# Kernel optimization log

Hardware: AMD Instinct MI355X
Metric: run time of the kernel (lower is better)

Reference implementation:

```python
import jax, jax.numpy as jnp
import numpy as np

STATE_DIM = 1024
INPUT_DIM = 1024
BATCH = 8192


def setup_inputs() -> dict:
    key = jax.random.key(0)
    ks = jax.random.split(key, 7)
    # Kaiming-uniform-ish init like torch Linear
    bx = 1.0 / np.sqrt(INPUT_DIM)
    bh = 1.0 / np.sqrt(STATE_DIM)
    return {
        "x": jax.random.normal(ks[0], (BATCH, INPUT_DIM), jnp.float32),
        "prevh": jax.random.normal(ks[1], (BATCH, STATE_DIM), jnp.float32),
        "prevc": jax.random.normal(ks[2], (BATCH, STATE_DIM), jnp.float32),
        "Wx": jax.random.uniform(ks[3], (INPUT_DIM, 4 * STATE_DIM), jnp.float32, -bx, bx),
        "bx": jax.random.uniform(ks[4], (4 * STATE_DIM,), jnp.float32, -bx, bx),
        "Wh": jax.random.uniform(ks[5], (STATE_DIM, 4 * STATE_DIM), jnp.float32, -bh, bh),
    }


def reference(x, prevh, prevc, Wx, bx, Wh):
    # stacked gate pre-activations: [B, 4*state_dim]
    stacked = x @ Wx + bx + prevh @ Wh
    i_bar, f_bar, o_bar, g_bar = jnp.split(stacked, 4, axis=1)
    i = jax.nn.sigmoid(i_bar)
    f = jax.nn.sigmoid(f_bar)
    o = jax.nn.sigmoid(o_bar)
    g = jnp.tanh(g_bar)
    nextc = prevc * f + g * i
    nexth = jnp.tanh(nextc) * o
    return (nexth, nextc)
```

## Files before the change

### kernel.cpp

```cpp
#include <hip/hip_runtime.h>
#include <hip/hip_bf16.h>


#define BATCH   8192
#define SDIM    1024
#define KDIM    2048
#define NT      32

typedef __attribute__((ext_vector_type(8))) short s16x8;
typedef __attribute__((ext_vector_type(4))) float f32x4;

__device__ __forceinline__ void gload16(const void* g, void* l) {
    __builtin_amdgcn_global_load_lds((const __attribute__((address_space(1))) void*)g,
                                     (__attribute__((address_space(3))) void*)l,
                                     16, 0, 0);
}

__device__ __forceinline__ float fast_sigmoid(float x) {
    return 1.0f / (1.0f + __expf(-x));
}
__device__ __forceinline__ float fast_tanh(float v) {
    float a = fabsf(v);
    float e = __expf(-2.0f * a);
    float t = (1.0f - e) / (1.0f + e);
    return copysignf(t, v);
}

__global__ __launch_bounds__(256) void convAW(
    const float* __restrict__ x,  const float* __restrict__ h,
    const float* __restrict__ Wx, const float* __restrict__ Wh,
    __hip_bfloat16* __restrict__ A, __hip_bfloat16* __restrict__ Wt)
{
    __shared__ float tile[64][68];
    if (blockIdx.x < 8192) {
        int t = blockIdx.x * 256 + threadIdx.x;
        int e = t << 3;
        int b = e >> 11;
        int k = e & 2047;
        const float* src = (k < 1024) ? (x + (size_t)b * 1024 + k)
                                      : (h + (size_t)b * 1024 + (k - 1024));
        float4 v0 = *(const float4*)(src);
        float4 v1 = *(const float4*)(src + 4);
        union { __hip_bfloat16 b[8]; s16x8 v; } u;
        u.b[0] = __float2bfloat16(v0.x); u.b[1] = __float2bfloat16(v0.y);
        u.b[2] = __float2bfloat16(v0.z); u.b[3] = __float2bfloat16(v0.w);
        u.b[4] = __float2bfloat16(v1.x); u.b[5] = __float2bfloat16(v1.y);
        u.b[6] = __float2bfloat16(v1.z); u.b[7] = __float2bfloat16(v1.w);
        *(s16x8*)(A + e) = u.v;
    } else {
        const int wb = blockIdx.x - 8192;
        const int kt = wb & 31;
        const int nt = wb >> 5;
        const int k0 = kt * 64, n0 = nt * 64;
        const int t  = threadIdx.x;

        {
            int r = t >> 2;
            int c = (t & 3) * 16;
            int k = k0 + r;
            const float* src = (k < 1024) ? (Wx + (size_t)k * 4096 + n0 + c)
                                          : (Wh + (size_t)(k - 1024) * 4096 + n0 + c);
#pragma unroll
            for (int jq = 0; jq < 4; ++jq)
                *(float4*)&tile[r][c + jq * 4] = *(const float4*)(src + jq * 4);
        }
        __syncthreads();

#pragma unroll
        for (int it = 0; it < 2; ++it) {
            int item = t + it * 256;
            int oct  = item >> 6;
            int nl   = item & 63;
            int n    = n0 + nl;
            int s    = n & 1023, g = n >> 10;
            int np   = (s >> 4) * 64 + g * 16 + (s & 15);
            union { __hip_bfloat16 b[8]; s16x8 v; } u;
#pragma unroll
            for (int e = 0; e < 8; ++e)
                u.b[e] = __float2bfloat16(tile[oct * 8 + e][nl]);
            *(s16x8*)(Wt + (size_t)np * 2048 + k0 + oct * 8) = u.v;
        }
    }
}

__global__ __launch_bounds__(512, 2) void lstm_gemm(
    const __hip_bfloat16* __restrict__ A,
    const __hip_bfloat16* __restrict__ Wt,
    const float* __restrict__ bx,
    const float* __restrict__ prevc,
    float* __restrict__ outh,
    float* __restrict__ outc)
{
    __shared__ __align__(16) char lds[131072];

    const int tid  = threadIdx.x;
    const int lane = tid & 63;
    const int w    = tid >> 6;
    const int wr   = w >> 2;
    const int wc   = w & 3;
    const int l15  = lane & 15;

    const int bid = blockIdx.x;
    const int xcd = bid & 7, j = bid >> 3;
    const int mt = (xcd >> 1) * 8 + (j & 7);
    const int nt = (xcd & 1) * 8 + (j >> 3);
    const int m0 = mt * 256, n0 = nt * 256, S0 = nt * 64;

    const int scol = ((lane & 7) ^ (lane >> 3)) << 3;
    const __hip_bfloat16* Ag = A  + (size_t)m0 * KDIM;
    const __hip_bfloat16* Bg = Wt + (size_t)n0 * KDIM;

    auto SA = [&](int tt, int p) {
        char* dst = lds + (2 * (tt & 1) + p) * 16384 + w * 1024;
        const __hip_bfloat16* src =
            Ag + (size_t)(p * 128 + w * 8 + (lane >> 3)) * KDIM + tt * 64 + scol;
        gload16(src, dst);
        gload16(src + (size_t)64 * KDIM, dst + 8192);
    };
    auto SB = [&](int tt, int p) {
        char* dst = lds + 65536 + (2 * (tt & 1) + p) * 16384 + w * 1024;
        const __hip_bfloat16* src =
            Bg + (size_t)(p * 128 + w * 8 + (lane >> 3)) * KDIM + tt * 64 + scol;
        gload16(src, dst);
        gload16(src + (size_t)64 * KDIM, dst + 8192);
    };

    f32x4 acc[8][4];
#pragma unroll
    for (int m = 0; m < 8; ++m)
#pragma unroll
        for (int g = 0; g < 4; ++g)
            acc[m][g] = (f32x4)0.0f;

    SB(0, 0); SB(0, 1); SA(0, 0); SA(0, 1); SB(1, 0); SB(1, 1);
    asm volatile("s_waitcnt vmcnt(4)" ::: "memory");
    __builtin_amdgcn_s_barrier();
    __builtin_amdgcn_sched_barrier(0);

    const int swz0 = (((lane >> 4))     ^ (lane & 7)) << 4;
    const int swz1 = (((lane >> 4) | 4) ^ (lane & 7)) << 4;
    const int brow = (wc & 1) * 64;

    s16x8 af[4][2], bf[4][2];

    for (int t = 0; t < NT; ++t) {
        const char* as = lds + (2 * (t & 1) + wr) * 16384;
        const char* bs = lds + 65536 + (2 * (t & 1) + (wc >> 1)) * 16384;

#pragma unroll
        for (int g = 0; g < 4; ++g) {
            bf[g][0] = *(const s16x8*)(bs + (brow + g * 16 + l15) * 128 + swz0);
            bf[g][1] = *(const s16x8*)(bs + (brow + g * 16 + l15) * 128 + swz1);
        }
#pragma unroll
        for (int m = 0; m < 4; ++m) {
            af[m][0] = *(const s16x8*)(as + (m * 16 + l15) * 128 + swz0);
            af[m][1] = *(const s16x8*)(as + (m * 16 + l15) * 128 + swz1);
        }
        if (t + 1 < NT) { SA(t + 1, 0); SA(t + 1, 1); }

        __builtin_amdgcn_s_setprio(1);
#pragma unroll
        for (int kf = 0; kf < 2; ++kf)
#pragma unroll
            for (int m = 0; m < 4; ++m)
#pragma unroll
                for (int g = 0; g < 4; ++g)
                    acc[m][g] = __builtin_amdgcn_mfma_f32_16x16x32_bf16(
                        af[m][kf], bf[g][kf], acc[m][g], 0, 0, 0);
        __builtin_amdgcn_s_setprio(0);

        __builtin_amdgcn_sched_barrier(0);
        __builtin_amdgcn_s_barrier();
        __builtin_amdgcn_sched_barrier(0);

#pragma unroll
        for (int m = 0; m < 4; ++m) {
            af[m][0] = *(const s16x8*)(as + ((m + 4) * 16 + l15) * 128 + swz0);
            af[m][1] = *(const s16x8*)(as + ((m + 4) * 16 + l15) * 128 + swz1);
        }
        if (t + 2 < NT) { SB(t + 2, 0); SB(t + 2, 1); }

        __builtin_amdgcn_s_setprio(1);
#pragma unroll
        for (int kf = 0; kf < 2; ++kf)
#pragma unroll
            for (int m = 0; m < 4; ++m)
#pragma unroll
                for (int g = 0; g < 4; ++g)
                    acc[m + 4][g] = __builtin_amdgcn_mfma_f32_16x16x32_bf16(
                        af[m][kf], bf[g][kf], acc[m + 4][g], 0, 0, 0);
        __builtin_amdgcn_s_setprio(0);

        __builtin_amdgcn_sched_barrier(0);
        if (t + 2 < NT) {
            asm volatile("s_waitcnt vmcnt(4)" ::: "memory");
        } else {
            asm volatile("s_waitcnt vmcnt(0)" ::: "memory");
        }
        __builtin_amdgcn_s_barrier();
        __builtin_amdgcn_sched_barrier(0);
    }

    const int st  = S0 + wc * 16 + l15;
    const float b_i = bx[st];
    const float b_f = bx[1024 + st];
    const float b_o = bx[2048 + st];
    const float b_g = bx[3072 + st];
    const int rbase = m0 + wr * 128 + (lane >> 4) * 4;

#pragma unroll
    for (int m = 0; m < 8; ++m) {
#pragma unroll
        for (int q = 0; q < 4; ++q) {
            int row = rbase + m * 16 + q;
            float ib = acc[m][0][q] + b_i;
            float fb = acc[m][1][q] + b_f;
            float ob = acc[m][2][q] + b_o;
            float gb = acc[m][3][q] + b_g;
            float ig = fast_sigmoid(ib);
            float fg = fast_sigmoid(fb);
            float og = fast_sigmoid(ob);
            float gg = fast_tanh(gb);
            float pc = prevc[(size_t)row * SDIM + st];
            float nc = pc * fg + gg * ig;
            float nh = fast_tanh(nc) * og;
            outh[(size_t)row * SDIM + st] = nh;
            outc[(size_t)row * SDIM + st] = nc;
        }
    }
}

extern "C" void kernel_launch(void* const* d_in, const int* in_sizes, int n_in,
                              void* d_out, int out_size, void* d_ws, size_t ws_size,
                              hipStream_t stream) {
    const float* x     = (const float*)d_in[0];
    const float* prevh = (const float*)d_in[1];
    const float* prevc = (const float*)d_in[2];
    const float* Wx    = (const float*)d_in[3];
    const float* bx    = (const float*)d_in[4];
    const float* Wh    = (const float*)d_in[5];

    __hip_bfloat16* Abf = (__hip_bfloat16*)d_ws;
    __hip_bfloat16* Wt  = Abf + (size_t)BATCH * KDIM;

    float* outh = (float*)d_out;
    float* outc = outh + (size_t)BATCH * SDIM;

    hipLaunchKernelGGL(convAW, dim3(10240), dim3(256), 0, stream,
                       x, prevh, Wx, Wh, Abf, Wt);
    hipLaunchKernelGGL(lstm_gemm, dim3(512), dim3(512), 0, stream,
                       Abf, Wt, bx, prevc, outh, outc);
}
```

Measured before the change: 156.1 us.

## Fuse activation fp32-to-bf16 conversion into GEMM A-tile loading

Drops the separate pass that converted x and prevh to a bf16 workspace matrix. The GEMM now loads fp32 activations straight into registers, converts them to bf16 and writes them into swizzled LDS, with the wait counts reorganised around this. This avoids writing and re-reading the 32MB bf16 copy of A. In exchange, A loads go through registers instead of direct global-to-LDS loads, fetch twice the bytes per tile (fp32) from global memory, and add conversion VALU work and extra waits inside the main loop.

```diff
diff --git a/kernel.cpp b/kernel.cpp
--- a/kernel.cpp
+++ b/kernel.cpp
@@ -26,65 +26,57 @@
     return copysignf(t, v);
 }
 
-__global__ __launch_bounds__(256) void convAW(
-    const float* __restrict__ x,  const float* __restrict__ h,
+__device__ __forceinline__ s16x8 cvt8(float4 a, float4 b) {
+    union { __hip_bfloat16 h[8]; s16x8 v; } u;
+    u.h[0] = __float2bfloat16(a.x); u.h[1] = __float2bfloat16(a.y);
+    u.h[2] = __float2bfloat16(a.z); u.h[3] = __float2bfloat16(a.w);
+    u.h[4] = __float2bfloat16(b.x); u.h[5] = __float2bfloat16(b.y);
+    u.h[6] = __float2bfloat16(b.z); u.h[7] = __float2bfloat16(b.w);
+    return u.v;
+}
+
+__global__ __launch_bounds__(256) void convW(
     const float* __restrict__ Wx, const float* __restrict__ Wh,
-    __hip_bfloat16* __restrict__ A, __hip_bfloat16* __restrict__ Wt)
+    __hip_bfloat16* __restrict__ Wt)
 {
     __shared__ float tile[64][68];
-    if (blockIdx.x < 8192) {
-        int t = blockIdx.x * 256 + threadIdx.x;
-        int e = t << 3;
-        int b = e >> 11;
-        int k = e & 2047;
-        const float* src = (k < 1024) ? (x + (size_t)b * 1024 + k)
-                                      : (h + (size_t)b * 1024 + (k - 1024));
-        float4 v0 = *(const float4*)(src);
-        float4 v1 = *(const float4*)(src + 4);
+    const int wb = blockIdx.x;
+    const int kt = wb & 31;
+    const int nt = wb >> 5;
+    const int k0 = kt * 64, n0 = nt * 64;
+    const int t  = threadIdx.x;
+
+    {
+        int r = t >> 2;
+        int c = (t & 3) * 16;
+        int k = k0 + r;
+        const float* src = (k < 1024) ? (Wx + (size_t)k * 4096 + n0 + c)
+                                      : (Wh + (size_t)(k - 1024) * 4096 + n0 + c);
+#pragma unroll
+        for (int jq = 0; jq < 4; ++jq)
+            *(float4*)&tile[r][c + jq * 4] = *(const float4*)(src + jq * 4);
+    }
+    __syncthreads();
+
+#pragma unroll
+    for (int it = 0; it < 2; ++it) {
+        int item = t + it * 256;
+        int oct  = item >> 6;
+        int nl   = item & 63;
+        int n    = n0 + nl;
+        int s    = n & 1023, g = n >> 10;
+        int np   = (s >> 4) * 64 + g * 16 + (s & 15);
         union { __hip_bfloat16 b[8]; s16x8 v; } u;
-        u.b[0] = __float2bfloat16(v0.x); u.b[1] = __float2bfloat16(v0.y);
-        u.b[2] = __float2bfloat16(v0.z); u.b[3] = __float2bfloat16(v0.w);
-        u.b[4] = __float2bfloat16(v1.x); u.b[5] = __float2bfloat16(v1.y);
-        u.b[6] = __float2bfloat16(v1.z); u.b[7] = __float2bfloat16(v1.w);
-        *(s16x8*)(A + e) = u.v;
-    } else {
-        const int wb = blockIdx.x - 8192;
-        const int kt = wb & 31;
-        const int nt = wb >> 5;
-        const int k0 = kt * 64, n0 = nt * 64;
-        const int t  = threadIdx.x;
-
-        {
-            int r = t >> 2;
-            int c = (t & 3) * 16;
-            int k = k0 + r;
-            const float* src = (k < 1024) ? (Wx + (size_t)k * 4096 + n0 + c)
-                                          : (Wh + (size_t)(k - 1024) * 4096 + n0 + c);
-#pragma unroll
-            for (int jq = 0; jq < 4; ++jq)
-                *(float4*)&tile[r][c + jq * 4] = *(const float4*)(src + jq * 4);
-        }
-        __syncthreads();
-
-#pragma unroll
-        for (int it = 0; it < 2; ++it) {
-            int item = t + it * 256;
-            int oct  = item >> 6;
-            int nl   = item & 63;
-            int n    = n0 + nl;
-            int s    = n & 1023, g = n >> 10;
-            int np   = (s >> 4) * 64 + g * 16 + (s & 15);
-            union { __hip_bfloat16 b[8]; s16x8 v; } u;
-#pragma unroll
-            for (int e = 0; e < 8; ++e)
-                u.b[e] = __float2bfloat16(tile[oct * 8 + e][nl]);
-            *(s16x8*)(Wt + (size_t)np * 2048 + k0 + oct * 8) = u.v;
-        }
+#pragma unroll
+        for (int e = 0; e < 8; ++e)
+            u.b[e] = __float2bfloat16(tile[oct * 8 + e][nl]);
+        *(s16x8*)(Wt + (size_t)np * 2048 + k0 + oct * 8) = u.v;
     }
 }
 
 __global__ __launch_bounds__(512, 2) void lstm_gemm(
-    const __hip_bfloat16* __restrict__ A,
+    const float* __restrict__ x,
+    const float* __restrict__ prevh,
     const __hip_bfloat16* __restrict__ Wt,
     const float* __restrict__ bx,
     const float* __restrict__ prevc,
@@ -107,16 +99,16 @@
     const int m0 = mt * 256, n0 = nt * 256, S0 = nt * 64;
 
     const int scol = ((lane & 7) ^ (lane >> 3)) << 3;
-    const __hip_bfloat16* Ag = A  + (size_t)m0 * KDIM;
     const __hip_bfloat16* Bg = Wt + (size_t)n0 * KDIM;
-
-    auto SA = [&](int tt, int p) {
-        char* dst = lds + (2 * (tt & 1) + p) * 16384 + w * 1024;
-        const __hip_bfloat16* src =
-            Ag + (size_t)(p * 128 + w * 8 + (lane >> 3)) * KDIM + tt * 64 + scol;
-        gload16(src, dst);
-        gload16(src + (size_t)64 * KDIM, dst + 8192);
+    const float* xg = x     + (size_t)m0 * 1024;
+    const float* hg = prevh + (size_t)m0 * 1024;
+    const int arow = w * 8 + (lane >> 3);
+
+    auto aptr = [&](int row, int tt) -> const float* {
+        return (tt < 16) ? xg + (size_t)row * 1024 + tt * 64 + scol
+                         : hg + (size_t)row * 1024 + (tt - 16) * 64 + scol;
     };
+
     auto SB = [&](int tt, int p) {
         char* dst = lds + 65536 + (2 * (tt & 1) + p) * 16384 + w * 1024;
         const __hip_bfloat16* src =
@@ -132,8 +124,36 @@
         for (int g = 0; g < 4; ++g)
             acc[m][g] = (f32x4)0.0f;
 
-    SB(0, 0); SB(0, 1); SA(0, 0); SA(0, 1); SB(1, 0); SB(1, 1);
-    asm volatile("s_waitcnt vmcnt(4)" ::: "memory");
+    float4 a00a, a00b, a01a, a01b, a10a, a10b, a11a, a11b;
+
+#define ALOAD(TT)                                                   \
+    {                                                               \
+        const float* q0 = aptr(arow, TT);                           \
+        const float* q1 = q0 + (size_t)64 * 1024;                   \
+        const float* q2 = aptr(arow + 128, TT);                     \
+        const float* q3 = q2 + (size_t)64 * 1024;                   \
+        a00a = *(const float4*)q0; a00b = *(const float4*)(q0 + 4); \
+        a01a = *(const float4*)q1; a01b = *(const float4*)(q1 + 4); \
+        a10a = *(const float4*)q2; a10b = *(const float4*)(q2 + 4); \
+        a11a = *(const float4*)q3; a11b = *(const float4*)(q3 + 4); \
+    }
+
+#define AWRITE(TT)                                                  \
+    {                                                               \
+        char* d0 = lds + (2 * ((TT) & 1)) * 16384 + w * 1024 + lane * 16; \
+        *(s16x8*)d0          = cvt8(a00a, a00b);                    \
+        *(s16x8*)(d0 + 8192) = cvt8(a01a, a01b);                    \
+        char* d1 = d0 + 16384;                                      \
+        *(s16x8*)d1          = cvt8(a10a, a10b);                    \
+        *(s16x8*)(d1 + 8192) = cvt8(a11a, a11b);                    \
+    }
+
+    ALOAD(0);
+    SB(0, 0); SB(0, 1); SB(1, 0); SB(1, 1);
+    asm volatile("s_waitcnt vmcnt(8)" ::: "memory");
+    __builtin_amdgcn_sched_barrier(0);
+    AWRITE(0);
+    asm volatile("s_waitcnt vmcnt(4) lgkmcnt(0)" ::: "memory");
     __builtin_amdgcn_s_barrier();
     __builtin_amdgcn_sched_barrier(0);
 
@@ -157,7 +177,7 @@
             af[m][0] = *(const s16x8*)(as + (m * 16 + l15) * 128 + swz0);
             af[m][1] = *(const s16x8*)(as + (m * 16 + l15) * 128 + swz1);
         }
-        if (t + 1 < NT) { SA(t + 1, 0); SA(t + 1, 1); }
+        if (t + 1 < NT) ALOAD(t + 1);
 
         __builtin_amdgcn_s_setprio(1);
 #pragma unroll
@@ -181,6 +201,16 @@
         }
         if (t + 2 < NT) { SB(t + 2, 0); SB(t + 2, 1); }
 
+        if (t + 2 < NT) {
+            asm volatile("s_waitcnt vmcnt(4)" ::: "memory");
+        } else if (t + 1 < NT) {
+            asm volatile("s_waitcnt vmcnt(0)" ::: "memory");
+        } else {
+            asm volatile("s_waitcnt vmcnt(0)" ::: "memory");
+        }
+        __builtin_amdgcn_sched_barrier(0);
+        if (t + 1 < NT) AWRITE(t + 1);
+
         __builtin_amdgcn_s_setprio(1);
 #pragma unroll
         for (int kf = 0; kf < 2; ++kf)
@@ -193,14 +223,12 @@
         __builtin_amdgcn_s_setprio(0);
 
         __builtin_amdgcn_sched_barrier(0);
-        if (t + 2 < NT) {
-            asm volatile("s_waitcnt vmcnt(4)" ::: "memory");
-        } else {
-            asm volatile("s_waitcnt vmcnt(0)" ::: "memory");
-        }
+        asm volatile("s_waitcnt lgkmcnt(0)" ::: "memory");
         __builtin_amdgcn_s_barrier();
         __builtin_amdgcn_sched_barrier(0);
     }
+#undef ALOAD
+#undef AWRITE
 
     const int st  = S0 + wc * 16 + l15;
     const float b_i = bx[st];
@@ -241,14 +269,12 @@
     const float* bx    = (const float*)d_in[4];
     const float* Wh    = (const float*)d_in[5];
 
-    __hip_bfloat16* Abf = (__hip_bfloat16*)d_ws;
-    __hip_bfloat16* Wt  = Abf + (size_t)BATCH * KDIM;
+    __hip_bfloat16* Wt = (__hip_bfloat16*)d_ws;
 
     float* outh = (float*)d_out;
     float* outc = outh + (size_t)BATCH * SDIM;
 
-    hipLaunchKernelGGL(convAW, dim3(10240), dim3(256), 0, stream,
-                       x, prevh, Wx, Wh, Abf, Wt);
+    hipLaunchKernelGGL(convW, dim3(2048), dim3(256), 0, stream, Wx, Wh, Wt);
     hipLaunchKernelGGL(lstm_gemm, dim3(512), dim3(512), 0, stream,
-                       Abf, Wt, bx, prevc, outh, outc);
-}
+                       x, prevh, Wt, bx, prevc, outh, outc);
+}
```

Measured after the change: 179.7 us. 15.1% more time.

## Shrink GEMM tile to 128x128 with K-step 32 and 256-thread blocks

Applied to the files above, without the earlier changes.

Replaces the 256x256 tile, 512-thread, K=64 GEMM with a 128x128 tile, 4 waves, K=32 per step and 32KB LDS. The grid grows to 2048 blocks with up to 3 blocks per CU, trading the larger tile's data reuse for occupancy and a simpler double-buffer pipeline. Each step now waits for all outstanding global loads before its barrier, which may expose load latency, and the smaller tile doubles the total traffic of A and W into LDS.

```diff
diff --git a/kernel.cpp b/kernel.cpp
--- a/kernel.cpp
+++ b/kernel.cpp
@@ -5,7 +5,7 @@
 #define BATCH   8192
 #define SDIM    1024
 #define KDIM    2048
-#define NT      32
+#define NT      64
 
 typedef __attribute__((ext_vector_type(8))) short s16x8;
 typedef __attribute__((ext_vector_type(4))) float f32x4;
@@ -53,7 +53,6 @@
         const int nt = wb >> 5;
         const int k0 = kt * 64, n0 = nt * 64;
         const int t  = threadIdx.x;
-
         {
             int r = t >> 2;
             int c = (t & 3) * 16;
@@ -65,7 +64,6 @@
                 *(float4*)&tile[r][c + jq * 4] = *(const float4*)(src + jq * 4);
         }
         __syncthreads();
-
 #pragma unroll
         for (int it = 0; it < 2; ++it) {
             int item = t + it * 256;
@@ -83,7 +81,7 @@
     }
 }
 
-__global__ __launch_bounds__(512, 2) void lstm_gemm(
+__global__ __launch_bounds__(256, 3) void lstm_gemm(
     const __hip_bfloat16* __restrict__ A,
     const __hip_bfloat16* __restrict__ Wt,
     const float* __restrict__ bx,
@@ -91,126 +89,101 @@
     float* __restrict__ outh,
     float* __restrict__ outc)
 {
-    __shared__ __align__(16) char lds[131072];
+    __shared__ __align__(16) char lds[32768];
 
     const int tid  = threadIdx.x;
     const int lane = tid & 63;
     const int w    = tid >> 6;
-    const int wr   = w >> 2;
-    const int wc   = w & 3;
+    const int wr   = w >> 1;
+    const int wc   = w & 1;
     const int l15  = lane & 15;
 
     const int bid = blockIdx.x;
     const int xcd = bid & 7, j = bid >> 3;
-    const int mt = (xcd >> 1) * 8 + (j & 7);
-    const int nt = (xcd & 1) * 8 + (j >> 3);
-    const int m0 = mt * 256, n0 = nt * 256, S0 = nt * 64;
-
-    const int scol = ((lane & 7) ^ (lane >> 3)) << 3;
+    const int mt  = (xcd >> 1) * 16 + (j & 15);
+    const int ntl = (xcd & 1) * 16 + (j >> 4);
+    const int m0  = mt * 128, n0 = ntl * 128;
+
+    const int gl    = (lane & 7) ^ (lane >> 3);
+    const int gl_hi = gl >> 2;
+    const int gl_k  = (gl & 3) * 8;
     const __hip_bfloat16* Ag = A  + (size_t)m0 * KDIM;
     const __hip_bfloat16* Bg = Wt + (size_t)n0 * KDIM;
 
-    auto SA = [&](int tt, int p) {
-        char* dst = lds + (2 * (tt & 1) + p) * 16384 + w * 1024;
-        const __hip_bfloat16* src =
-            Ag + (size_t)(p * 128 + w * 8 + (lane >> 3)) * KDIM + tt * 64 + scol;
-        gload16(src, dst);
-        gload16(src + (size_t)64 * KDIM, dst + 8192);
+    auto SA = [&](int tt) {
+        char* dst = lds + (tt & 1) * 8192 + w * 1024;
+#pragma unroll
+        for (int r = 0; r < 2; ++r) {
+            int row = 2 * (r * 32 + w * 8 + (lane >> 3)) + gl_hi;
+            gload16(Ag + (size_t)row * KDIM + tt * 32 + gl_k, dst + r * 4096);
+        }
     };
-    auto SB = [&](int tt, int p) {
-        char* dst = lds + 65536 + (2 * (tt & 1) + p) * 16384 + w * 1024;
-        const __hip_bfloat16* src =
-            Bg + (size_t)(p * 128 + w * 8 + (lane >> 3)) * KDIM + tt * 64 + scol;
-        gload16(src, dst);
-        gload16(src + (size_t)64 * KDIM, dst + 8192);
+    auto SB = [&](int tt) {
+        char* dst = lds + 16384 + (tt & 1) * 8192 + w * 1024;
+#pragma unroll
+        for (int r = 0; r < 2; ++r) {
+            int row = 2 * (r * 32 + w * 8 + (lane >> 3)) + gl_hi;
+            gload16(Bg + (size_t)row * KDIM + tt * 32 + gl_k, dst + r * 4096);
+        }
     };
 
-    f32x4 acc[8][4];
-#pragma unroll
-    for (int m = 0; m < 8; ++m)
+    f32x4 acc[4][4];
+#pragma unroll
+    for (int m = 0; m < 4; ++m)
 #pragma unroll
         for (int g = 0; g < 4; ++g)
             acc[m][g] = (f32x4)0.0f;
 
-    SB(0, 0); SB(0, 1); SA(0, 0); SA(0, 1); SB(1, 0); SB(1, 1);
-    asm volatile("s_waitcnt vmcnt(4)" ::: "memory");
+    SA(0); SB(0);
+    asm volatile("s_waitcnt vmcnt(0)" ::: "memory");
     __builtin_amdgcn_s_barrier();
     __builtin_amdgcn_sched_barrier(0);
 
-    const int swz0 = (((lane >> 4))     ^ (lane & 7)) << 4;
-    const int swz1 = (((lane >> 4) | 4) ^ (lane & 7)) << 4;
-    const int brow = (wc & 1) * 64;
-
-    s16x8 af[4][2], bf[4][2];
+    const int rdoff = ((l15 >> 1) << 7)
+                    + (((((l15 & 1) << 2) | (lane >> 4)) ^ (l15 >> 1)) << 4);
+    const int abase = wr * 32 * 128;
+    const int bbase = wc * 32 * 128;
+
+    s16x8 af[4], bf[4];
 
     for (int t = 0; t < NT; ++t) {
-        const char* as = lds + (2 * (t & 1) + wr) * 16384;
-        const char* bs = lds + 65536 + (2 * (t & 1) + (wc >> 1)) * 16384;
-
-#pragma unroll
-        for (int g = 0; g < 4; ++g) {
-            bf[g][0] = *(const s16x8*)(bs + (brow + g * 16 + l15) * 128 + swz0);
-            bf[g][1] = *(const s16x8*)(bs + (brow + g * 16 + l15) * 128 + swz1);
-        }
-#pragma unroll
-        for (int m = 0; m < 4; ++m) {
-            af[m][0] = *(const s16x8*)(as + (m * 16 + l15) * 128 + swz0);
-            af[m][1] = *(const s16x8*)(as + (m * 16 + l15) * 128 + swz1);
-        }
-        if (t + 1 < NT) { SA(t + 1, 0); SA(t + 1, 1); }
-
+        const char* as = lds + (t & 1) * 8192;
+        const char* bs = lds + 16384 + (t & 1) * 8192;
+
+#pragma unroll
+        for (int g = 0; g < 4; ++g)
+            bf[g] = *(const s16x8*)(bs + bbase + g * 1024 + rdoff);
+#pragma unroll
+        for (int m = 0; m < 4; ++m)
+            af[m] = *(const s16x8*)(as + abase + m * 1024 + rdoff);
+
+        if (t + 1 < NT) { SA(t + 1); SB(t + 1); }
+
+        asm volatile("s_waitcnt lgkmcnt(0)" ::: "memory");
+        __builtin_amdgcn_sched_barrier(0);
         __builtin_amdgcn_s_setprio(1);
 #pragma unroll
-        for (int kf = 0; kf < 2; ++kf)
-#pragma unroll
-            for (int m = 0; m < 4; ++m)
-#pragma unroll
-                for (int g = 0; g < 4; ++g)
-                    acc[m][g] = __builtin_amdgcn_mfma_f32_16x16x32_bf16(
-                        af[m][kf], bf[g][kf], acc[m][g], 0, 0, 0);
+        for (int m = 0; m < 4; ++m)
+#pragma unroll
+            for (int g = 0; g < 4; ++g)
+                acc[m][g] = __builtin_amdgcn_mfma_f32_16x16x32_bf16(
+                    af[m], bf[g], acc[m][g], 0, 0, 0);
         __builtin_amdgcn_s_setprio(0);
 
-        __builtin_amdgcn_sched_barrier(0);
-        __builtin_amdgcn_s_barrier();
-        __builtin_amdgcn_sched_barrier(0);
-
-#pragma unroll
-        for (int m = 0; m < 4; ++m) {
-            af[m][0] = *(const s16x8*)(as + ((m + 4) * 16 + l15) * 128 + swz0);
-            af[m][1] = *(const s16x8*)(as + ((m + 4) * 16 + l15) * 128 + swz1);
-        }
-        if (t + 2 < NT) { SB(t + 2, 0); SB(t + 2, 1); }
-
-        __builtin_amdgcn_s_setprio(1);
-#pragma unroll
-        for (int kf = 0; kf < 2; ++kf)
-#pragma unroll
-            for (int m = 0; m < 4; ++m)
-#pragma unroll
-                for (int g = 0; g < 4; ++g)
-                    acc[m + 4][g] = __builtin_amdgcn_mfma_f32_16x16x32_bf16(
-                        af[m][kf], bf[g][kf], acc[m + 4][g], 0, 0, 0);
-        __builtin_amdgcn_s_setprio(0);
-
-        __builtin_amdgcn_sched_barrier(0);
-        if (t + 2 < NT) {
-            asm volatile("s_waitcnt vmcnt(4)" ::: "memory");
-        } else {
-            asm volatile("s_waitcnt vmcnt(0)" ::: "memory");
-        }
+        asm volatile("s_waitcnt vmcnt(0)" ::: "memory");
         __builtin_amdgcn_s_barrier();
         __builtin_amdgcn_sched_barrier(0);
     }
 
-    const int st  = S0 + wc * 16 + l15;
+    const int st  = ntl * 32 + wc * 16 + l15;
     const float b_i = bx[st];
     const float b_f = bx[1024 + st];
     const float b_o = bx[2048 + st];
     const float b_g = bx[3072 + st];
-    const int rbase = m0 + wr * 128 + (lane >> 4) * 4;
-
-#pragma unroll
-    for (int m = 0; m < 8; ++m) {
+    const int rbase = m0 + wr * 64 + (lane >> 4) * 4;
+
+#pragma unroll
+    for (int m = 0; m < 4; ++m) {
 #pragma unroll
         for (int q = 0; q < 4; ++q) {
             int row = rbase + m * 16 + q;
@@ -249,6 +222,6 @@
 
     hipLaunchKernelGGL(convAW, dim3(10240), dim3(256), 0, stream,
                        x, prevh, Wx, Wh, Abf, Wt);
-    hipLaunchKernelGGL(lstm_gemm, dim3(512), dim3(512), 0, stream,
+    hipLaunchKernelGGL(lstm_gemm, dim3(2048), dim3(256), 0, stream,
                        Abf, Wt, bx, prevc, outh, outc);
 }
```

Result: slower. 190.9 us (+22.3%).
